# Kernel tuning notes

Hardware: AMD Instinct MI355X
Metric: run time of the kernel (lower is better)

Reference implementation:

```python
import jax, jax.numpy as jnp
import numpy as np

S, O, A, R = 32, 64, 8, 8   # s_nvals, o_nvals, a_nvals, r_nvals
B, T = 1024, 128            # batch of episodes, n_transitions


def setup_inputs() -> dict:
    key = jax.random.key(0)
    ks = jax.random.split(key, 10)
    regime = jax.random.randint(ks[0], (B,), 0, 2).astype(jnp.float32)
    obs = jax.random.randint(ks[1], (T + 1, B), 0, O)
    rewards = jax.random.randint(ks[2], (T + 1, B), 0, R)
    dones = (jax.random.uniform(ks[3], (T + 1, B)) < 0.02).astype(jnp.float32)
    actions = jax.random.randint(ks[4], (T, B), 0, A)
    params_s = jax.random.normal(ks[5], (S,), dtype=jnp.float32)
    params_s_sa = jax.random.normal(ks[6], (S, A, S), dtype=jnp.float32)
    params_o_s = jax.random.normal(ks[7], (S, O), dtype=jnp.float32)
    params_r_s = jax.random.normal(ks[8], (S, R), dtype=jnp.float32)
    params_a_s = jax.random.normal(ks[9], (S, A), dtype=jnp.float32)
    return {
        "regime": regime, "obs": obs, "rewards": rewards, "dones": dones,
        "actions": actions, "params_s": params_s, "params_s_sa": params_s_sa,
        "params_o_s": params_o_s, "params_r_s": params_r_s, "params_a_s": params_a_s,
    }


def _log_prob(regime, obs, rewards, dones, actions,
              params_s, params_s_sa, params_o_s, params_r_s, params_a_s):
    """Batched HMM forward-filtering log p(o_{0:T}, r_{0:T}, a_{0:T-1}) (with_done=False)."""
    log_pi = jax.nn.log_softmax(params_s, axis=-1)      # [S]
    log_Tr = jax.nn.log_softmax(params_s_sa, axis=-1)   # [S, A, S']
    log_Os = jax.nn.log_softmax(params_o_s, axis=-1)    # [S, O]
    log_Rs = jax.nn.log_softmax(params_r_s, axis=-1)    # [S, R]
    log_As = jax.nn.log_softmax(params_a_s, axis=-1)    # [S, A]
    log_Tr_a = jnp.transpose(log_Tr, (1, 0, 2))          # [A, S, S']
    Bsz = regime.shape[0]
    regime_mask = (regime == 1.0)[:, None]               # [B, 1]

    def step(carry, xs):
        log_q_s_hprev, log_prob, was_done = carry        # [B,S], [B], [B]
        o, r, d, a = xs                                  # each [B]
        done = jnp.maximum(was_done, d)
        log_q_o = log_Os.T[o]                            # [B, S]
        log_q_r = log_Rs.T[r]                            # [B, S]
        log_q_a = log_As.T[a]                            # [B, S]
        log_q_a = jnp.where((done == 1.0)[:, None] | regime_mask, 0.0, log_q_a)
        log_q_sorda = log_q_s_hprev + log_q_o + log_q_r + log_q_a   # [B, S]
        log_q_orda = jax.nn.logsumexp(log_q_sorda, axis=-1) * (1.0 - was_done)
        log_prob = jnp.where(jnp.isinf(log_prob), log_prob, log_prob + log_q_orda)
        log_q_s_h = log_q_sorda - log_q_orda[:, None]    # posterior over s_t, [B, S]
        # predict: logsumexp over s of q(s|h) * p(s'|s,a)  -> [B, S']
        log_q_snext = jax.nn.logsumexp(log_q_s_h[:, :, None] + log_Tr_a[a], axis=1)
        return (log_q_snext, log_prob, done), None

    init = (jnp.broadcast_to(log_pi, (Bsz, S)),
            jnp.zeros((Bsz,), log_pi.dtype),
            jnp.zeros((Bsz,), dones.dtype))
    (log_q_s_hprev, log_prob, was_done), _ = jax.lax.scan(
        step, init, (obs[:-1], rewards[:-1], dones[:-1], actions))

    # final step t = T: no action term, no transition
    log_q_sord = log_q_s_hprev + log_Os.T[obs[-1]] + log_Rs.T[rewards[-1]]
    log_q_ord = jax.nn.logsumexp(log_q_sord, axis=-1) * (1.0 - was_done)
    log_prob = jnp.where(jnp.isinf(log_prob), log_prob, log_prob + log_q_ord)
    return log_prob


def reference(regime, obs, rewards, dones, actions,
              params_s, params_s_sa, params_o_s, params_r_s, params_a_s):
    return _log_prob(regime, obs, rewards, dones, actions,
                     params_s, params_s_sa, params_o_s, params_r_s, params_a_s)
```

## Files before the change

kernel.cpp:

```cpp
#include <hip/hip_runtime.h>

#define S_N 32
#define O_N 64
#define A_N 8
#define R_N 8
#define B_N 1024
#define T_N 128

#define L_OT 0
#define L_RA 2048
#define L_RT 4096
#define L_PI 4352
#define L_N  4384

typedef float f32x4 __attribute__((ext_vector_type(4)));
typedef short bf16x8 __attribute__((ext_vector_type(8)));

#define RLI(v, l) __builtin_amdgcn_readlane((v), (l))

#define LOADT(TH0, TH1, A_) {                                                \
    const bf16x8* p_ = reinterpret_cast<const bf16x8*>(sTH + ((A_) << 7));   \
    TH0 = p_[lane];                                                          \
    TH1 = p_[lane + 64]; }

#define LOADE(ELO, EHI, PKW) {                                               \
    const unsigned pk_ = (PKW);                                              \
    const int ob_ = L_OT + (int)(pk_ & 63u) * 32 + h0;                       \
    const int rb_ = eBase + (int)((pk_ >> 6) & 7u) * eMulR                   \
                  + (int)((pk_ >> 9) & 7u) * eMulA + h0;                     \
    ELO = sE[ob_] * sE[rb_];                                                 \
    EHI = sE[ob_ + 16] * sE[rb_ + 16]; }

#define STEP(ELO, EHI, TH0, TH1) {                                           \
    const float wlo = ulo * (ELO), whi = uhi * (EHI);                        \
    const int ilo = __float_as_int(wlo) + 0x8000;                            \
    const int ihi = __float_as_int(whi) + 0x8000;                            \
    const int pw = (int)(((unsigned)ilo >> 16) | ((unsigned)ihi & 0xffff0000u)); \
    union { int i[4]; bf16x8 v; } A_;                                        \
    A_.i[0] = __builtin_amdgcn_ds_bpermute(bpb,      pw);                    \
    A_.i[1] = __builtin_amdgcn_ds_bpermute(bpb + 4,  pw);                    \
    A_.i[2] = __builtin_amdgcn_ds_bpermute(bpb + 8,  pw);                    \
    A_.i[3] = __builtin_amdgcn_ds_bpermute(bpb + 12, pw);                    \
    const f32x4 d0 = __builtin_amdgcn_mfma_f32_16x16x32_bf16(A_.v, TH0, zf4, 0, 0, 0); \
    const f32x4 d1 = __builtin_amdgcn_mfma_f32_16x16x32_bf16(A_.v, TH1, zf4, 0, 0, 0); \
    ulo = d0[0]; uhi = d1[0];                                                \
}

#define RESCALE() {                                                          \
    const int ub = RLI(__float_as_int(ulo), 0);                              \
    const int kb = (ub >> 23) & 255;                                         \
    const float sc_ = __int_as_float((254 - kb) << 23);                      \
    ulo *= sc_; uhi *= sc_;                                                  \
    ksum += kb - 127; }

__global__ __launch_bounds__(256) void tam_fused(
    const float* __restrict__ regime,
    const int*   __restrict__ obs,
    const int*   __restrict__ rewards,
    const int*   __restrict__ dones_i,
    const int*   __restrict__ actions,
    const float* __restrict__ params_s,
    const float* __restrict__ params_s_sa,
    const float* __restrict__ params_o_s,
    const float* __restrict__ params_r_s,
    const float* __restrict__ params_a_s,
    float* __restrict__ out)
{
    __shared__ uint4 sTH[1024];
    __shared__ float sE[L_N];
    __shared__ float sAT[256];
    const int tid  = threadIdx.x;
    const int lane = tid & 63;
    const int wid  = tid >> 6;
    const int h0   = lane & 15;
    const int g    = lane >> 4;
    const int bpb  = g * 16;
    const int b    = blockIdx.x * 4 + wid;
    const f32x4 zf4 = {0.f, 0.f, 0.f, 0.f};

    if (tid < 128) {
        unsigned short* sTHh = reinterpret_cast<unsigned short*>(sTH);
        #pragma unroll 1
        for (int rr = 0; rr < 2; ++rr) {
            const int idx = 2 * tid + rr;
            const int s = idx >> 3, a = idx & 7;
            const float* row = params_s_sa + (s * A_N + a) * S_N;
            float p[32];
            #pragma unroll
            for (int i = 0; i < 8; ++i) {
                float4 v = reinterpret_cast<const float4*>(row)[i];
                p[4*i]=v.x; p[4*i+1]=v.y; p[4*i+2]=v.z; p[4*i+3]=v.w;
            }
            float mx = p[0];
            #pragma unroll
            for (int i = 1; i < 32; ++i) mx = fmaxf(mx, p[i]);
            float sum = 0.f;
            #pragma unroll
            for (int i = 0; i < 32; ++i) { p[i] = __expf(p[i] - mx); sum += p[i]; }
            const float inv = 1.0f / sum;
            const int ks = 2 * (s & 15) + (s >> 4);
            const int gk = ks >> 3, e8 = ks & 7;
            #pragma unroll
            for (int d = 0; d < 32; ++d) {
                const unsigned bits = __float_as_uint(p[d] * inv) + 0x8000u;
                const int l2 = 16 * gk + (d & 15);
                sTHh[((a * 2 + (d >> 4)) * 64 + l2) * 8 + e8] =
                    (unsigned short)(bits >> 16);
            }
        }
    } else {
        const int e = tid - 128;
        if (e < 32) {
            const int s = e;
            const float* row = params_o_s + s * O_N;
            float p[64];
            #pragma unroll
            for (int i = 0; i < 16; ++i) {
                float4 v = reinterpret_cast<const float4*>(row)[i];
                p[4*i]=v.x; p[4*i+1]=v.y; p[4*i+2]=v.z; p[4*i+3]=v.w;
            }
            float mx = p[0];
            #pragma unroll
            for (int i = 1; i < 64; ++i) mx = fmaxf(mx, p[i]);
            float sum = 0.f;
            #pragma unroll
            for (int i = 0; i < 64; ++i) { p[i] = __expf(p[i] - mx); sum += p[i]; }
            const float inv = 1.0f / sum;
            #pragma unroll
            for (int o = 0; o < 64; ++o) sE[L_OT + o * 32 + s] = p[o] * inv;
        } else if (e < 64) {
            const int s = e - 32;
            const float* row = params_r_s + s * R_N;
            float p[8];
            #pragma unroll
            for (int i = 0; i < 2; ++i) {
                float4 v = reinterpret_cast<const float4*>(row)[i];
                p[4*i]=v.x; p[4*i+1]=v.y; p[4*i+2]=v.z; p[4*i+3]=v.w;
            }
            float mx = p[0];
            #pragma unroll
            for (int i = 1; i < 8; ++i) mx = fmaxf(mx, p[i]);
            float sum = 0.f;
            #pragma unroll
            for (int i = 0; i < 8; ++i) { p[i] = __expf(p[i] - mx); sum += p[i]; }
            const float inv = 1.0f / sum;
            #pragma unroll
            for (int r = 0; r < 8; ++r) sE[L_RT + r * 32 + s] = p[r] * inv;
        } else if (e < 96) {
            const int s = e - 64;
            const float* row = params_a_s + s * A_N;
            float p[8];
            #pragma unroll
            for (int i = 0; i < 2; ++i) {
                float4 v = reinterpret_cast<const float4*>(row)[i];
                p[4*i]=v.x; p[4*i+1]=v.y; p[4*i+2]=v.z; p[4*i+3]=v.w;
            }
            float mx = p[0];
            #pragma unroll
            for (int i = 1; i < 8; ++i) mx = fmaxf(mx, p[i]);
            float sum = 0.f;
            #pragma unroll
            for (int i = 0; i < 8; ++i) { p[i] = __expf(p[i] - mx); sum += p[i]; }
            const float inv = 1.0f / sum;
            #pragma unroll
            for (int a = 0; a < 8; ++a) sAT[a * 32 + s] = p[a] * inv;
        } else {
            const int s = e - 96;
            float p[32];
            #pragma unroll
            for (int i = 0; i < 8; ++i) {
                float4 v = reinterpret_cast<const float4*>(params_s)[i];
                p[4*i]=v.x; p[4*i+1]=v.y; p[4*i+2]=v.z; p[4*i+3]=v.w;
            }
            float mx = p[0];
            #pragma unroll
            for (int i = 1; i < 32; ++i) mx = fmaxf(mx, p[i]);
            float sum = 0.f;
            #pragma unroll
            for (int i = 0; i < 32; ++i) { p[i] = __expf(p[i] - mx); sum += p[i]; }
            sE[L_PI + s] = p[s] / sum;
        }
    }
    __syncthreads();
    #pragma unroll 1
    for (int i = tid; i < 2048; i += 256) {
        const int sl2 = i & 31, ra = i >> 5;
        sE[L_RA + i] = sE[L_RT + (ra >> 3) * 32 + sl2] * sAT[(ra & 7) * 32 + sl2];
    }
    __syncthreads();

    const int t0 = 2 * lane, t1 = 2 * lane + 1;
    const int o0 = obs[t0 * B_N + b],      o1 = obs[t1 * B_N + b];
    const int r0 = rewards[t0 * B_N + b],  r1 = rewards[t1 * B_N + b];
    const int a0 = actions[t0 * B_N + b],  a1 = actions[t1 * B_N + b];
    const int d0i = dones_i[t0 * B_N + b], d1i = dones_i[t1 * B_N + b];
    const int vpk = (o0 | (r0 << 6) | (a0 << 9)) |
                    ((o1 | (r1 << 6) | (a1 << 9)) << 16);

    const unsigned long long mEv = __ballot(d0i != 0);
    const unsigned long long mOd = __ballot(d1i != 0);
    const int tE = mEv ? 2 * __builtin_ctzll(mEv)     : (1 << 30);
    const int tO = mOd ? 2 * __builtin_ctzll(mOd) + 1 : (1 << 30);
    const int tstar  = tE < tO ? tE : tO;
    const int nsteps = tstar < 128 ? tstar : 128;

    const bool skipA = (regime[b] == 1.0f);
    const int eBase = skipA ? L_RT : L_RA;
    const int eMulR = skipA ? 32 : 256;
    const int eMulA = skipA ? 0 : 32;

    float ulo = sE[L_PI + h0];
    float uhi = sE[L_PI + h0 + 16];
    int ksum = 0;
    float eloA, ehiA, eloB, ehiB;
    bf16x8 thA0, thA1, thB0, thB1;

    unsigned pkc = (unsigned)RLI(vpk, 0);
    unsigned pkn = (unsigned)RLI(vpk, 1);
    LOADE(eloA, ehiA, pkc & 0xffffu);
    LOADT(thA0, thA1, (int)((pkc >> 9) & 7u));

    const int npairs = nsteps >> 1;
    #pragma unroll 1
    for (int i = 0; i < npairs; ++i) {
        LOADE(eloB, ehiB, pkc >> 16);
        LOADT(thB0, thB1, (int)((pkc >> 25) & 7u));
        STEP(eloA, ehiA, thA0, thA1);
        LOADE(eloA, ehiA, pkn & 0xffffu);
        LOADT(thA0, thA1, (int)((pkn >> 9) & 7u));
        STEP(eloB, ehiB, thB0, thB1);
        pkc = pkn;
        pkn = (unsigned)RLI(vpk, i + 2);
        RESCALE();
    }

    if (nsteps & 1) {
        STEP(eloA, ehiA, thA0, thA1);
    }

    {
        const int e  = nsteps;
        const int oe = obs[e * B_N + b];
        const int re = rewards[e * B_N + b];
        const int ob = L_OT + oe * 32 + h0;
        const int rb = L_RT + re * 32 + h0;
        float t = ulo * sE[ob] * sE[rb] + uhi * sE[ob + 16] * sE[rb + 16];
        t += __shfl_xor(t, 1, 16);
        t += __shfl_xor(t, 2, 16);
        t += __shfl_xor(t, 4, 16);
        t += __shfl_xor(t, 8, 16);
        const float result = (float)ksum * 0.69314718055994531f + __logf(t);
        if (lane == 0) out[b] = result;
    }
}

extern "C" void kernel_launch(void* const* d_in, const int* in_sizes, int n_in,
                              void* d_out, int out_size, void* d_ws, size_t ws_size,
                              hipStream_t stream) {
    (void)in_sizes; (void)n_in; (void)out_size; (void)d_ws; (void)ws_size;
    const float* regime      = (const float*)d_in[0];
    const int*   obs         = (const int*)d_in[1];
    const int*   rewards     = (const int*)d_in[2];
    const int*   dones_i     = (const int*)d_in[3];
    const int*   actions     = (const int*)d_in[4];
    const float* params_s    = (const float*)d_in[5];
    const float* params_s_sa = (const float*)d_in[6];
    const float* params_o_s  = (const float*)d_in[7];
    const float* params_r_s  = (const float*)d_in[8];
    const float* params_a_s  = (const float*)d_in[9];
    float* out = (float*)d_out;

    tam_fused<<<256, 256, 0, stream>>>(regime, obs, rewards, dones_i, actions,
                                       params_s, params_s_sa, params_o_s,
                                       params_r_s, params_a_s, out);
}
```

Measured before the change: 26.33 us.

## Precompute combined two-step transition matrices off the serial chain

For each pair of steps, the kernel now builds the product T(a1)·diag(emission2)·T(a2) with MFMAs. This work does not depend on the recurrence, so it can overlap with the chain. The dependent chain then does one MFMA step per two timesteps instead of two, which shortens the serial latency path. It adds extra MFMA work and LDS traffic per step (a float copy of the transition table), uses packed bf16 conversion, and moves rescaling into the next emission. The bf16 rounding of the intermediate product could slightly change accuracy.

```diff
diff --git a/kernel.cpp b/kernel.cpp
--- a/kernel.cpp
+++ b/kernel.cpp
@@ -18,12 +18,15 @@
 
 #define RLI(v, l) __builtin_amdgcn_readlane((v), (l))
 
-#define LOADT(TH0, TH1, A_) {                                                \
-    const bf16x8* p_ = reinterpret_cast<const bf16x8*>(sTH + ((A_) << 7));   \
-    TH0 = p_[lane];                                                          \
-    TH1 = p_[lane + 64]; }
-
-#define LOADE(ELO, EHI, PKW) {                                               \
+static __device__ __forceinline__ int cvtpk(float lo, float hi) {
+    int r;
+    asm("v_cvt_pk_bf16_f32 %0, %1, %2" : "=v"(r) : "v"(lo), "v"(hi));
+    return r;
+}
+
+union U8 { int i[4]; bf16x8 v; };
+
+#define LOADE1(ELO, EHI, PKW) {                                              \
     const unsigned pk_ = (PKW);                                              \
     const int ob_ = L_OT + (int)(pk_ & 63u) * 32 + h0;                       \
     const int rb_ = eBase + (int)((pk_ >> 6) & 7u) * eMulR                   \
@@ -31,27 +34,54 @@
     ELO = sE[ob_] * sE[rb_];                                                 \
     EHI = sE[ob_ + 16] * sE[rb_ + 16]; }
 
-#define STEP(ELO, EHI, TH0, TH1) {                                           \
-    const float wlo = ulo * (ELO), whi = uhi * (EHI);                        \
-    const int ilo = __float_as_int(wlo) + 0x8000;                            \
-    const int ihi = __float_as_int(whi) + 0x8000;                            \
-    const int pw = (int)(((unsigned)ilo >> 16) | ((unsigned)ihi & 0xffff0000u)); \
-    union { int i[4]; bf16x8 v; } A_;                                        \
-    A_.i[0] = __builtin_amdgcn_ds_bpermute(bpb,      pw);                    \
-    A_.i[1] = __builtin_amdgcn_ds_bpermute(bpb + 4,  pw);                    \
-    A_.i[2] = __builtin_amdgcn_ds_bpermute(bpb + 8,  pw);                    \
-    A_.i[3] = __builtin_amdgcn_ds_bpermute(bpb + 12, pw);                    \
-    const f32x4 d0 = __builtin_amdgcn_mfma_f32_16x16x32_bf16(A_.v, TH0, zf4, 0, 0, 0); \
-    const f32x4 d1 = __builtin_amdgcn_mfma_f32_16x16x32_bf16(A_.v, TH1, zf4, 0, 0, 0); \
-    ulo = d0[0]; uhi = d1[0];                                                \
-}
-
-#define RESCALE() {                                                          \
-    const int ub = RLI(__float_as_int(ulo), 0);                              \
-    const int kb = (ub >> 23) & 255;                                         \
-    const float sc_ = __int_as_float((254 - kb) << 23);                      \
-    ulo *= sc_; uhi *= sc_;                                                  \
-    ksum += kb - 127; }
+#define BUILDP(PKW, B0, B1) {                                                \
+    const unsigned pk_ = (PKW);                                              \
+    const int a1_ = (int)((pk_ >> 9) & 7u);                                  \
+    const int o2_ = (int)((pk_ >> 16) & 63u);                                \
+    const int a2_ = (int)((pk_ >> 25) & 7u);                                 \
+    const int eb2_ = eBase + (int)((pk_ >> 22) & 7u) * eMulR + a2_ * eMulA;  \
+    const float4 otl_ = *reinterpret_cast<const float4*>(sE + L_OT + o2_*32 + 4*g); \
+    const float4 oth_ = *reinterpret_cast<const float4*>(sE + L_OT + o2_*32 + 4*g + 16); \
+    const float4 ral_ = *reinterpret_cast<const float4*>(sE + eb2_ + 4*g);   \
+    const float4 rah_ = *reinterpret_cast<const float4*>(sE + eb2_ + 4*g + 16); \
+    const bf16x8* pta_ = reinterpret_cast<const bf16x8*>(sTA) + a1_*128 + lane; \
+    const bf16x8 ta0_ = pta_[0], ta1_ = pta_[64];                            \
+    const float4* ptb_ = reinterpret_cast<const float4*>(sTB) + (a2_*128 + lane)*2; \
+    const float4 b0a_ = ptb_[0], b0b_ = ptb_[1];                             \
+    const float4 b1a_ = ptb_[128], b1b_ = ptb_[129];                         \
+    const float e20_ = otl_.x*ral_.x, e21_ = oth_.x*rah_.x;                  \
+    const float e22_ = otl_.y*ral_.y, e23_ = oth_.y*rah_.y;                  \
+    const float e24_ = otl_.z*ral_.z, e25_ = oth_.z*rah_.z;                  \
+    const float e26_ = otl_.w*ral_.w, e27_ = oth_.w*rah_.w;                  \
+    U8 bp0_, bp1_;                                                           \
+    bp0_.i[0] = cvtpk(b0a_.x*e20_, b0a_.y*e21_);                             \
+    bp0_.i[1] = cvtpk(b0a_.z*e22_, b0a_.w*e23_);                             \
+    bp0_.i[2] = cvtpk(b0b_.x*e24_, b0b_.y*e25_);                             \
+    bp0_.i[3] = cvtpk(b0b_.z*e26_, b0b_.w*e27_);                             \
+    bp1_.i[0] = cvtpk(b1a_.x*e20_, b1a_.y*e21_);                             \
+    bp1_.i[1] = cvtpk(b1a_.z*e22_, b1a_.w*e23_);                             \
+    bp1_.i[2] = cvtpk(b1b_.x*e24_, b1b_.y*e25_);                             \
+    bp1_.i[3] = cvtpk(b1b_.z*e26_, b1b_.w*e27_);                             \
+    const f32x4 D00_ = __builtin_amdgcn_mfma_f32_16x16x32_bf16(ta0_, bp0_.v, zf4, 0,0,0); \
+    const f32x4 D10_ = __builtin_amdgcn_mfma_f32_16x16x32_bf16(ta1_, bp0_.v, zf4, 0,0,0); \
+    const f32x4 D01_ = __builtin_amdgcn_mfma_f32_16x16x32_bf16(ta0_, bp1_.v, zf4, 0,0,0); \
+    const f32x4 D11_ = __builtin_amdgcn_mfma_f32_16x16x32_bf16(ta1_, bp1_.v, zf4, 0,0,0); \
+    (B0).i[0] = cvtpk(D00_[0], D10_[0]); (B0).i[1] = cvtpk(D00_[1], D10_[1]); \
+    (B0).i[2] = cvtpk(D00_[2], D10_[2]); (B0).i[3] = cvtpk(D00_[3], D10_[3]); \
+    (B1).i[0] = cvtpk(D01_[0], D11_[0]); (B1).i[1] = cvtpk(D01_[1], D11_[1]); \
+    (B1).i[2] = cvtpk(D01_[2], D11_[2]); (B1).i[3] = cvtpk(D01_[3], D11_[3]); }
+
+#define CHAINSTEP(E1LO, E1HI, BB0, BB1) {                                    \
+    const float wlo_ = ulo * (E1LO), whi_ = uhi * (E1HI);                    \
+    const int pw_ = cvtpk(wlo_, whi_);                                       \
+    U8 Aw_;                                                                  \
+    Aw_.i[0] = __builtin_amdgcn_ds_bpermute(bpb,      pw_);                  \
+    Aw_.i[1] = __builtin_amdgcn_ds_bpermute(bpb + 4,  pw_);                  \
+    Aw_.i[2] = __builtin_amdgcn_ds_bpermute(bpb + 8,  pw_);                  \
+    Aw_.i[3] = __builtin_amdgcn_ds_bpermute(bpb + 12, pw_);                  \
+    const f32x4 d0_ = __builtin_amdgcn_mfma_f32_16x16x32_bf16(Aw_.v, (BB0).v, zf4, 0,0,0); \
+    const f32x4 d1_ = __builtin_amdgcn_mfma_f32_16x16x32_bf16(Aw_.v, (BB1).v, zf4, 0,0,0); \
+    ulo = d0_[0]; uhi = d1_[0]; }
 
 __global__ __launch_bounds__(256) void tam_fused(
     const float* __restrict__ regime,
@@ -66,8 +96,9 @@
     const float* __restrict__ params_a_s,
     float* __restrict__ out)
 {
-    __shared__ uint4 sTH[1024];
-    __shared__ float sE[L_N];
+    __shared__ __align__(16) unsigned short sTA[8192];
+    __shared__ __align__(16) float sTB[8192];
+    __shared__ __align__(16) float sE[L_N];
     __shared__ float sAT[256];
     const int tid  = threadIdx.x;
     const int lane = tid & 63;
@@ -79,7 +110,6 @@
     const f32x4 zf4 = {0.f, 0.f, 0.f, 0.f};
 
     if (tid < 128) {
-        unsigned short* sTHh = reinterpret_cast<unsigned short*>(sTH);
         #pragma unroll 1
         for (int rr = 0; rr < 2; ++rr) {
             const int idx = 2 * tid + rr;
@@ -98,15 +128,25 @@
             #pragma unroll
             for (int i = 0; i < 32; ++i) { p[i] = __expf(p[i] - mx); sum += p[i]; }
             const float inv = 1.0f / sum;
-            const int ks = 2 * (s & 15) + (s >> 4);
-            const int gk = ks >> 3, e8 = ks & 7;
-            #pragma unroll
-            for (int d = 0; d < 32; ++d) {
-                const unsigned bits = __float_as_uint(p[d] * inv) + 0x8000u;
-                const int l2 = 16 * gk + (d & 15);
-                sTHh[((a * 2 + (d >> 4)) * 64 + l2) * 8 + e8] =
-                    (unsigned short)(bits >> 16);
-            }
+            const int h = s >> 4, rlow = s & 15;
+            #pragma unroll
+            for (int gg = 0; gg < 4; ++gg) {
+                #pragma unroll
+                for (int j = 0; j < 8; ++j) {
+                    const int dst = 4*gg + (j >> 1) + ((j & 1) << 4);
+                    const unsigned bits = __float_as_uint(p[dst] * inv) + 0x8000u;
+                    sTA[((a*2 + h)*64 + 16*gg + rlow)*8 + j] =
+                        (unsigned short)(bits >> 16);
+                }
+            }
+            int gs, js;
+            if (s < 16) { gs = s >> 2; js = 2 * (s & 3); }
+            else        { gs = (s - 16) >> 2; js = 2 * ((s - 16) & 3) + 1; }
+            #pragma unroll
+            for (int f = 0; f < 2; ++f)
+                #pragma unroll
+                for (int c = 0; c < 16; ++c)
+                    sTB[((a*2 + f)*64 + 16*gs + c)*8 + js] = p[c + 16*f] * inv;
         }
     } else {
         const int e = tid - 128;
@@ -212,30 +252,44 @@
     float ulo = sE[L_PI + h0];
     float uhi = sE[L_PI + h0 + 16];
     int ksum = 0;
-    float eloA, ehiA, eloB, ehiB;
-    bf16x8 thA0, thA1, thB0, thB1;
+    float scp = 1.0f;
+
+    U8 B0c, B1c, B0n, B1n;
+    float e1clo, e1chi, e1nlo, e1nhi;
 
     unsigned pkc = (unsigned)RLI(vpk, 0);
     unsigned pkn = (unsigned)RLI(vpk, 1);
-    LOADE(eloA, ehiA, pkc & 0xffffu);
-    LOADT(thA0, thA1, (int)((pkc >> 9) & 7u));
+    LOADE1(e1clo, e1chi, pkc);
+    BUILDP(pkc, B0c, B1c);
 
     const int npairs = nsteps >> 1;
     #pragma unroll 1
     for (int i = 0; i < npairs; ++i) {
-        LOADE(eloB, ehiB, pkc >> 16);
-        LOADT(thB0, thB1, (int)((pkc >> 25) & 7u));
-        STEP(eloA, ehiA, thA0, thA1);
-        LOADE(eloA, ehiA, pkn & 0xffffu);
-        LOADT(thA0, thA1, (int)((pkn >> 9) & 7u));
-        STEP(eloB, ehiB, thB0, thB1);
+        LOADE1(e1nlo, e1nhi, pkn);
+        BUILDP(pkn, B0n, B1n);
+        CHAINSTEP(e1clo, e1chi, B0c, B1c);
+        const int kb = (RLI(__float_as_int(ulo), 0) >> 23) & 255;
+        scp = __int_as_float((254 - kb) << 23);
+        ksum += kb - 127;
+        e1nlo *= scp; e1nhi *= scp;
+        B0c = B0n; B1c = B1n; e1clo = e1nlo; e1chi = e1nhi;
         pkc = pkn;
         pkn = (unsigned)RLI(vpk, i + 2);
-        RESCALE();
     }
 
     if (nsteps & 1) {
-        STEP(eloA, ehiA, thA0, thA1);
+        const int a1s = (int)((pkc >> 9) & 7u);
+        const float4* ptb = reinterpret_cast<const float4*>(sTB) + (a1s*128 + lane)*2;
+        const float4 s0a = ptb[0], s0b = ptb[1];
+        const float4 s1a = ptb[128], s1b = ptb[129];
+        U8 Bs0, Bs1;
+        Bs0.i[0] = cvtpk(s0a.x, s0a.y); Bs0.i[1] = cvtpk(s0a.z, s0a.w);
+        Bs0.i[2] = cvtpk(s0b.x, s0b.y); Bs0.i[3] = cvtpk(s0b.z, s0b.w);
+        Bs1.i[0] = cvtpk(s1a.x, s1a.y); Bs1.i[1] = cvtpk(s1a.z, s1a.w);
+        Bs1.i[2] = cvtpk(s1b.x, s1b.y); Bs1.i[3] = cvtpk(s1b.z, s1b.w);
+        CHAINSTEP(e1clo, e1chi, Bs0, Bs1);
+    } else {
+        ulo *= scp; uhi *= scp;
     }
 
     {
```

Result: slower. 30.21 us (+14.7%).

## Transpose MFMA operands to remove per-step bpermute and fold rescale into emission

Applied to the files above, without the earlier changes.

Swaps the MFMA operand roles so the transition matrix is the A operand and the belief vector is B. Each lane then owns four consecutive states of the output, which can be packed straight into the next step's B operand with v_cvt_pk_bf16_f32 instead of four ds_bpermute cross-lane shuffles per step. Emission factors are loaded as float4 vectors, and the power-of-two rescale is folded into the emission multiply on every step rather than every other step. The loop becomes a single per-step loop with a deferred ksum update and a different final reduction. This trades an extra multiply per element and a readlane per step for removing the LDS permute latency from the serial dependency chain.

```diff
diff --git a/kernel.cpp b/kernel.cpp
--- a/kernel.cpp
+++ b/kernel.cpp
@@ -18,40 +18,13 @@
 
 #define RLI(v, l) __builtin_amdgcn_readlane((v), (l))
 
-#define LOADT(TH0, TH1, A_) {                                                \
-    const bf16x8* p_ = reinterpret_cast<const bf16x8*>(sTH + ((A_) << 7));   \
-    TH0 = p_[lane];                                                          \
-    TH1 = p_[lane + 64]; }
-
-#define LOADE(ELO, EHI, PKW) {                                               \
-    const unsigned pk_ = (PKW);                                              \
-    const int ob_ = L_OT + (int)(pk_ & 63u) * 32 + h0;                       \
-    const int rb_ = eBase + (int)((pk_ >> 6) & 7u) * eMulR                   \
-                  + (int)((pk_ >> 9) & 7u) * eMulA + h0;                     \
-    ELO = sE[ob_] * sE[rb_];                                                 \
-    EHI = sE[ob_ + 16] * sE[rb_ + 16]; }
-
-#define STEP(ELO, EHI, TH0, TH1) {                                           \
-    const float wlo = ulo * (ELO), whi = uhi * (EHI);                        \
-    const int ilo = __float_as_int(wlo) + 0x8000;                            \
-    const int ihi = __float_as_int(whi) + 0x8000;                            \
-    const int pw = (int)(((unsigned)ilo >> 16) | ((unsigned)ihi & 0xffff0000u)); \
-    union { int i[4]; bf16x8 v; } A_;                                        \
-    A_.i[0] = __builtin_amdgcn_ds_bpermute(bpb,      pw);                    \
-    A_.i[1] = __builtin_amdgcn_ds_bpermute(bpb + 4,  pw);                    \
-    A_.i[2] = __builtin_amdgcn_ds_bpermute(bpb + 8,  pw);                    \
-    A_.i[3] = __builtin_amdgcn_ds_bpermute(bpb + 12, pw);                    \
-    const f32x4 d0 = __builtin_amdgcn_mfma_f32_16x16x32_bf16(A_.v, TH0, zf4, 0, 0, 0); \
-    const f32x4 d1 = __builtin_amdgcn_mfma_f32_16x16x32_bf16(A_.v, TH1, zf4, 0, 0, 0); \
-    ulo = d0[0]; uhi = d1[0];                                                \
+static __device__ __forceinline__ int cvtpk(float lo, float hi) {
+    int r;
+    asm("v_cvt_pk_bf16_f32 %0, %1, %2" : "=v"(r) : "v"(lo), "v"(hi));
+    return r;
 }
 
-#define RESCALE() {                                                          \
-    const int ub = RLI(__float_as_int(ulo), 0);                              \
-    const int kb = (ub >> 23) & 255;                                         \
-    const float sc_ = __int_as_float((254 - kb) << 23);                      \
-    ulo *= sc_; uhi *= sc_;                                                  \
-    ksum += kb - 127; }
+union U8 { int i[4]; bf16x8 v; };
 
 __global__ __launch_bounds__(256) void tam_fused(
     const float* __restrict__ regime,
@@ -66,15 +39,15 @@
     const float* __restrict__ params_a_s,
     float* __restrict__ out)
 {
-    __shared__ uint4 sTH[1024];
-    __shared__ float sE[L_N];
+    __shared__ __align__(16) uint4 sTH[1024];
+    __shared__ __align__(16) float sE[L_N];
     __shared__ float sAT[256];
     const int tid  = threadIdx.x;
     const int lane = tid & 63;
     const int wid  = tid >> 6;
-    const int h0   = lane & 15;
     const int g    = lane >> 4;
-    const int bpb  = g * 16;
+    const int c0   = 4 * g;
+    const int c1   = 4 * g + 16;
     const int b    = blockIdx.x * 4 + wid;
     const f32x4 zf4 = {0.f, 0.f, 0.f, 0.f};
 
@@ -209,47 +182,82 @@
     const int eMulR = skipA ? 32 : 256;
     const int eMulA = skipA ? 0 : 32;
 
-    float ulo = sE[L_PI + h0];
-    float uhi = sE[L_PI + h0 + 16];
-    int ksum = 0;
-    float eloA, ehiA, eloB, ehiB;
-    bf16x8 thA0, thA1, thB0, thB1;
+    float scp = 1.0f;
+    int kpend = 0, ksum = 0;
+    f32x4 D1, D2;
+    U8 B;
+    bf16x8 tAc0, tAc1;
 
     unsigned pkc = (unsigned)RLI(vpk, 0);
     unsigned pkn = (unsigned)RLI(vpk, 1);
-    LOADE(eloA, ehiA, pkc & 0xffffu);
-    LOADT(thA0, thA1, (int)((pkc >> 9) & 7u));
-
-    const int npairs = nsteps >> 1;
+
+    {
+        const float4 piL = *(const float4*)(sE + L_PI + c0);
+        const float4 piH = *(const float4*)(sE + L_PI + c1);
+        D1[0]=piL.x; D1[1]=piL.y; D1[2]=piL.z; D1[3]=piL.w;
+        D2[0]=piH.x; D2[1]=piH.y; D2[2]=piH.z; D2[3]=piH.w;
+        const unsigned f0 = pkc & 0xffffu;
+        const int a0f = (int)((f0 >> 9) & 7u);
+        const int ob_ = L_OT + (int)(f0 & 63u) * 32;
+        const int rb_ = eBase + (int)((f0 >> 6) & 7u) * eMulR + a0f * eMulA;
+        const float4 oL = *(const float4*)(sE + ob_ + c0);
+        const float4 oH = *(const float4*)(sE + ob_ + c1);
+        const float4 rL = *(const float4*)(sE + rb_ + c0);
+        const float4 rH = *(const float4*)(sE + rb_ + c1);
+        B.i[0] = cvtpk(D1[0]*oL.x*rL.x, D2[0]*oH.x*rH.x);
+        B.i[1] = cvtpk(D1[1]*oL.y*rL.y, D2[1]*oH.y*rH.y);
+        B.i[2] = cvtpk(D1[2]*oL.z*rL.z, D2[2]*oH.z*rH.z);
+        B.i[3] = cvtpk(D1[3]*oL.w*rL.w, D2[3]*oH.w*rH.w);
+        const bf16x8* pA_ = reinterpret_cast<const bf16x8*>(sTH) + a0f * 128 + lane;
+        tAc0 = pA_[0]; tAc1 = pA_[64];
+    }
+
     #pragma unroll 1
-    for (int i = 0; i < npairs; ++i) {
-        LOADE(eloB, ehiB, pkc >> 16);
-        LOADT(thB0, thB1, (int)((pkc >> 25) & 7u));
-        STEP(eloA, ehiA, thA0, thA1);
-        LOADE(eloA, ehiA, pkn & 0xffffu);
-        LOADT(thA0, thA1, (int)((pkn >> 9) & 7u));
-        STEP(eloB, ehiB, thB0, thB1);
-        pkc = pkn;
-        pkn = (unsigned)RLI(vpk, i + 2);
-        RESCALE();
-    }
-
-    if (nsteps & 1) {
-        STEP(eloA, ehiA, thA0, thA1);
+    for (int t = 0; t < nsteps; ++t) {
+        const unsigned f1 = (t & 1) ? (pkn & 0xffffu) : (pkc >> 16);
+        const int a1f = (int)((f1 >> 9) & 7u);
+        const bf16x8* pA_ = reinterpret_cast<const bf16x8*>(sTH) + a1f * 128 + lane;
+        const bf16x8 tAn0 = pA_[0], tAn1 = pA_[64];
+        const int ob_ = L_OT + (int)(f1 & 63u) * 32;
+        const int rb_ = eBase + (int)((f1 >> 6) & 7u) * eMulR + a1f * eMulA;
+        const float4 oL = *(const float4*)(sE + ob_ + c0);
+        const float4 oH = *(const float4*)(sE + ob_ + c1);
+        const float4 rL = *(const float4*)(sE + rb_ + c0);
+        const float4 rH = *(const float4*)(sE + rb_ + c1);
+        D1 = __builtin_amdgcn_mfma_f32_16x16x32_bf16(tAc0, B.v, zf4, 0, 0, 0);
+        D2 = __builtin_amdgcn_mfma_f32_16x16x32_bf16(tAc1, B.v, zf4, 0, 0, 0);
+        ksum += (t + 1 < nsteps) ? kpend : 0;
+        const float eL0 = oL.x*rL.x*scp, eL1 = oL.y*rL.y*scp,
+                    eL2 = oL.z*rL.z*scp, eL3 = oL.w*rL.w*scp;
+        const float eH0 = oH.x*rH.x*scp, eH1 = oH.y*rH.y*scp,
+                    eH2 = oH.z*rH.z*scp, eH3 = oH.w*rH.w*scp;
+        B.i[0] = cvtpk(D1[0]*eL0, D2[0]*eH0);
+        B.i[1] = cvtpk(D1[1]*eL1, D2[1]*eH1);
+        B.i[2] = cvtpk(D1[2]*eL2, D2[2]*eH2);
+        B.i[3] = cvtpk(D1[3]*eL3, D2[3]*eH3);
+        const int kb = (RLI(__float_as_int(D1[0]), 0) >> 23) & 255;
+        kpend = kb - 127;
+        scp = __int_as_float((254 - kb) << 23);
+        tAc0 = tAn0; tAc1 = tAn1;
+        const unsigned nw = (unsigned)RLI(vpk, (t >> 1) + 2);
+        if (t & 1) { pkc = pkn; pkn = nw; }
     }
 
     {
         const int e  = nsteps;
         const int oe = obs[e * B_N + b];
         const int re = rewards[e * B_N + b];
-        const int ob = L_OT + oe * 32 + h0;
-        const int rb = L_RT + re * 32 + h0;
-        float t = ulo * sE[ob] * sE[rb] + uhi * sE[ob + 16] * sE[rb + 16];
-        t += __shfl_xor(t, 1, 16);
-        t += __shfl_xor(t, 2, 16);
-        t += __shfl_xor(t, 4, 16);
-        t += __shfl_xor(t, 8, 16);
-        const float result = (float)ksum * 0.69314718055994531f + __logf(t);
+        const float4 oL = *(const float4*)(sE + L_OT + oe * 32 + c0);
+        const float4 oH = *(const float4*)(sE + L_OT + oe * 32 + c1);
+        const float4 rL = *(const float4*)(sE + L_RT + re * 32 + c0);
+        const float4 rH = *(const float4*)(sE + L_RT + re * 32 + c1);
+        float tq = D1[0]*oL.x*rL.x + D1[1]*oL.y*rL.y
+                 + D1[2]*oL.z*rL.z + D1[3]*oL.w*rL.w
+                 + D2[0]*oH.x*rH.x + D2[1]*oH.y*rH.y
+                 + D2[2]*oH.z*rH.z + D2[3]*oH.w*rH.w;
+        tq += __shfl_xor(tq, 16);
+        tq += __shfl_xor(tq, 32);
+        const float result = (float)ksum * 0.69314718055994531f + __logf(tq);
         if (lane == 0) out[b] = result;
     }
 }
```

Result: slower. 34.11 us (+29.6%).
